# Kernel optimization log

Hardware: AMD Instinct MI355X
Metric: run time of the kernel (lower is better)

## Reference

```python
import jax, jax.numpy as jnp
import numpy as np

H, KV, D = 16, 4, 128
WIN = 512
EPS = 1e-6


def rms_norm(x, w):
    # x: [..., D]
    return x * jax.lax.rsqrt(jnp.mean(x * x, axis=-1, keepdims=True) + EPS) * w


def rotate_half(x):
    x1, x2 = jnp.split(x, 2, axis=-1)
    return jnp.concatenate([-x2, x1], axis=-1)


def setup_inputs() -> dict:
    key = jax.random.key(0)
    ks = jax.random.split(key, 8)
    B, L, hidden = 2, 2048, 2048
    x = jax.random.normal(ks[0], (B, L, hidden), jnp.float32)
    # realistic RoPE tables
    inv_freq = 1.0 / (10000.0 ** (np.arange(0, D, 2, dtype=np.float32) / D))
    t = np.arange(L, dtype=np.float32)
    freqs = np.outer(t, inv_freq)  # [L, D/2]
    emb = np.concatenate([freqs, freqs], axis=-1)  # [L, D]
    cos = jnp.asarray(np.cos(emb), jnp.float32)
    sin = jnp.asarray(np.sin(emb), jnp.float32)
    s = 0.02
    Wq = jax.random.normal(ks[1], (H * D, hidden), jnp.float32) * s
    Wk = jax.random.normal(ks[2], (KV * D, hidden), jnp.float32) * s
    Wv = jax.random.normal(ks[3], (KV * D, hidden), jnp.float32) * s
    Wo = jax.random.normal(ks[4], (hidden, H * D), jnp.float32) * s
    q_norm_w = jnp.ones((D,), jnp.float32)
    k_norm_w = jnp.ones((D,), jnp.float32)
    return {"x": x, "cos": cos, "sin": sin, "Wq": Wq, "Wk": Wk, "Wv": Wv,
            "Wo": Wo, "q_norm_w": q_norm_w, "k_norm_w": k_norm_w}


def reference(x, cos, sin, Wq, Wk, Wv, Wo, q_norm_w, k_norm_w):
    B, L, _ = x.shape
    # projections (torch Linear: y = x @ W.T)
    q = (x @ Wq.T).reshape(B, L, H, D)
    k = (x @ Wk.T).reshape(B, L, KV, D)
    v = (x @ Wv.T).reshape(B, L, KV, D)
    # QK RMSNorm, then [B, heads, L, D]
    q = jnp.transpose(rms_norm(q, q_norm_w), (0, 2, 1, 3))
    k = jnp.transpose(rms_norm(k, k_norm_w), (0, 2, 1, 3))
    v = jnp.transpose(v, (0, 2, 1, 3))
    # RoPE
    c = cos[None, None]  # [1,1,L,D]
    s = sin[None, None]
    q = q * c + rotate_half(q) * s
    k = k * c + rotate_half(k) * s
    # GQA repeat_interleave over head dim
    n_rep = H // KV
    k = jnp.repeat(k, n_rep, axis=1)
    v = jnp.repeat(v, n_rep, axis=1)
    # sliding-window additive bias [L, L]
    idx = jnp.arange(L)
    in_win = jnp.abs(idx[:, None] - idx[None, :]) <= WIN
    bias = jnp.where(in_win, 0.0, jnp.finfo(x.dtype).min).astype(x.dtype)
    # SDPA
    scale = 1.0 / jnp.sqrt(jnp.asarray(D, x.dtype))
    scores = jnp.einsum('bhqd,bhkd->bhqk', q, k) * scale + bias[None, None]
    attn = jax.nn.softmax(scores, axis=-1)
    out = jnp.einsum('bhqk,bhkd->bhqd', attn, v)  # [B,H,L,D]
    out = jnp.transpose(out, (0, 2, 1, 3)).reshape(B, L, H * D)
    return out @ Wo.T
```

## Files before the change

kernel.cpp:

```cpp
#include <hip/hip_runtime.h>
#include <hip/hip_bf16.h>


typedef unsigned short u16;
typedef unsigned int u32;
typedef __attribute__((ext_vector_type(8))) short bf16x8;
typedef __attribute__((ext_vector_type(4))) float f32x4;

#define AS1 __attribute__((address_space(1)))
#define AS3 __attribute__((address_space(3)))

__device__ __forceinline__ u16 f2b(float f) {
  union { float f; u32 u; } c; c.f = f;
  return (u16)((c.u + 0x8000u) >> 16);
}
__device__ __forceinline__ float b2f(u16 u) {
  union { u32 u; float f; } c; c.u = ((u32)u) << 16; return c.f;
}

__global__ __launch_bounds__(256) void cvt_all(const float* __restrict__ x,
                                               const float* __restrict__ wq,
                                               const float* __restrict__ wk,
                                               const float* __restrict__ wv,
                                               const float* __restrict__ wo,
                                               u16* __restrict__ xb,
                                               u16* __restrict__ wqkvb,
                                               u16* __restrict__ wob) {
  int blk = blockIdx.x;
  const float* s; u16* d; int off;
  if (blk < 8192)       { s = x;  d = xb;              off = blk * 1024; }
  else if (blk < 12288) { s = wq; d = wqkvb;           off = (blk - 8192) * 1024; }
  else if (blk < 13312) { s = wk; d = wqkvb + 4194304; off = (blk - 12288) * 1024; }
  else if (blk < 14336) { s = wv; d = wqkvb + 5242880; off = (blk - 13312) * 1024; }
  else                  { s = wo; d = wob;             off = (blk - 14336) * 1024; }
  int i = off + threadIdx.x * 4;
  float4 v = *(const float4*)(s + i);
  ushort4 o;
  o.x = f2b(v.x); o.y = f2b(v.y); o.z = f2b(v.z); o.w = f2b(v.w);
  *(ushort4*)(d + i) = o;
}

template<int F32OUT>
__global__ __launch_bounds__(256) void gemm_bt(const u16* __restrict__ A,
                                               const u16* __restrict__ Bm,
                                               void* __restrict__ C,
                                               int M, int N, int K) {
  __shared__ u16 As[128][64];
  __shared__ u16 Bs[128][64];
  const int tid  = threadIdx.x;
  const int w    = tid >> 6, lane = tid & 63, quad = lane >> 4, l16 = lane & 15;
  const int wm   = w >> 1, wn = w & 1;
  const int m0   = blockIdx.y * 128, n0 = blockIdx.x * 128;

  f32x4 zero = {0.f, 0.f, 0.f, 0.f};
  f32x4 acc[4][4];
#pragma unroll
  for (int i = 0; i < 4; i++)
#pragma unroll
    for (int j = 0; j < 4; j++) acc[i][j] = zero;

  const int srow = lane >> 3;
  const int swz8 = ((lane & 7) ^ (lane >> 3)) * 8;

  for (int k0 = 0; k0 < K; k0 += 64) {
#pragma unroll
    for (int p = 0; p < 4; ++p) {
      int row = p * 32 + w * 8 + srow;
      __builtin_amdgcn_global_load_lds(
          (const AS1 void*)(A + (size_t)(m0 + row) * K + k0 + swz8),
          (AS3 void*)((char*)&As[0][0] + p * 4096 + w * 1024), 16, 0, 0);
      __builtin_amdgcn_global_load_lds(
          (const AS1 void*)(Bm + (size_t)(n0 + row) * K + k0 + swz8),
          (AS3 void*)((char*)&Bs[0][0] + p * 4096 + w * 1024), 16, 0, 0);
    }
    __syncthreads();
#pragma unroll
    for (int kk = 0; kk < 64; kk += 32) {
      const int cs = ((kk >> 3) + quad) ^ (l16 & 7);
      bf16x8 af[4], bfr[4];
#pragma unroll
      for (int i = 0; i < 4; i++)
        af[i] = *(const bf16x8*)((const char*)&As[0][0] +
                                 (wm * 64 + i * 16 + l16) * 128 + cs * 16);
#pragma unroll
      for (int j = 0; j < 4; j++)
        bfr[j] = *(const bf16x8*)((const char*)&Bs[0][0] +
                                  (wn * 64 + j * 16 + l16) * 128 + cs * 16);
#pragma unroll
      for (int i = 0; i < 4; i++)
#pragma unroll
        for (int j = 0; j < 4; j++)
          acc[i][j] = __builtin_amdgcn_mfma_f32_16x16x32_bf16(af[i], bfr[j], acc[i][j], 0, 0, 0);
    }
    __syncthreads();
  }

#pragma unroll
  for (int i = 0; i < 4; i++) {
#pragma unroll
    for (int r = 0; r < 4; r++) {
      int gr = m0 + wm * 64 + i * 16 + quad * 4 + r;
#pragma unroll
      for (int j = 0; j < 4; j++) {
        int gc = n0 + wn * 64 + j * 16 + l16;
        if (F32OUT) ((float*)C)[(size_t)gr * N + gc] = acc[i][j][r];
        else        ((u16*)C)[(size_t)gr * N + gc]   = f2b(acc[i][j][r]);
      }
    }
  }
}

__global__ __launch_bounds__(256) void rmsrope(const u16* __restrict__ qkv,
                                               const float* __restrict__ cosT,
                                               const float* __restrict__ sinT,
                                               const float* __restrict__ qw,
                                               const float* __restrict__ kw,
                                               u16* __restrict__ qo,
                                               u16* __restrict__ ko) {
  int wid  = blockIdx.x * 4 + (threadIdx.x >> 6);
  int lane = threadIdx.x & 63;
  int r  = wid / 20;
  int hh = wid % 20;
  int b = r >> 11, l = r & 2047;
  int cb = hh < 16 ? hh * 128 : 2048 + (hh - 16) * 128;
  const u16* src = qkv + (size_t)r * 3072 + cb;
  float v0 = b2f(src[lane]);
  float v1 = b2f(src[lane + 64]);
  float ss = v0 * v0 + v1 * v1;
#pragma unroll
  for (int off = 1; off < 64; off <<= 1) ss += __shfl_xor(ss, off, 64);
  float inv = rsqrtf(ss * (1.0f / 128.0f) + 1e-6f);
  const float* wt = hh < 16 ? qw : kw;
  float n0 = v0 * inv * wt[lane];
  float n1 = v1 * inv * wt[lane + 64];
  float c0 = cosT[l * 128 + lane],      c1 = cosT[l * 128 + 64 + lane];
  float s0 = sinT[l * 128 + lane],      s1 = sinT[l * 128 + 64 + lane];
  float o0 = n0 * c0 - n1 * s0;
  float o1 = n1 * c1 + n0 * s1;
  const float qscale = 0.08838834764831845f * 1.4426950408889634f;
  u16* dst; size_t base;
  if (hh < 16) { dst = qo; base = ((size_t)(b * 16 + hh) * 2048 + l) * 128;
                 o0 *= qscale; o1 *= qscale; }
  else         { dst = ko; base = ((size_t)(b * 4 + (hh - 16)) * 2048 + l) * 128; }
  dst[base + lane]      = f2b(o0);
  dst[base + 64 + lane] = f2b(o1);
}

__global__ __launch_bounds__(256) void transpose_v(const u16* __restrict__ qkv,
                                                   u16* __restrict__ dst) {
  __shared__ u16 T[64][72];
  const int lt = blockIdx.x, dt = blockIdx.y, bh = blockIdx.z;
  const int b = bh >> 2, kv = bh & 3;
  const u16* s = qkv + ((size_t)(b * 2048 + lt * 64)) * 3072 + 2560 + kv * 128 + dt * 64;
  u16*       d = dst + (size_t)bh * 128 * 2048 + (size_t)dt * 64 * 2048 + lt * 64;
  const int t = threadIdx.x;
  const int row = t >> 3, c8 = (t & 7) * 8;
#pragma unroll
  for (int p = 0; p < 2; ++p)
    *(uint4*)&T[p * 32 + row][c8] = *(const uint4*)(s + (size_t)(p * 32 + row) * 3072 + c8);
  __syncthreads();
#pragma unroll
  for (int p = 0; p < 2; ++p) {
    int dr = p * 32 + row;
    u16 o[8];
#pragma unroll
    for (int j = 0; j < 8; ++j) o[j] = T[c8 + j][dr];
    *(uint4*)(d + (size_t)dr * 2048 + c8) = *(uint4*)o;
  }
}

__global__ __launch_bounds__(256) void flash_swa(const u16* __restrict__ Q,
                                                 const u16* __restrict__ Kg,
                                                 const u16* __restrict__ VTg,
                                                 u16* __restrict__ Og) {
  constexpr int L = 2048, D = 128;
  __shared__ u16 Ks[64][136];
  __shared__ u16 Vt[128][72];
  __shared__ u16 Ps[4][16][72];

  const int q0  = blockIdx.x * 128;
  const int h   = blockIdx.y;
  const int b   = blockIdx.z;
  const int tid = threadIdx.x;
  const int w = tid >> 6, lane = tid & 63, quad = lane >> 4, l16 = lane & 15;
  const int kvh = h >> 2;

  const u16* Qb  = Q   + (size_t)(b * 16 + h)  * L * D;
  const u16* Kb  = Kg  + (size_t)(b * 4 + kvh) * L * D;
  const u16* VTb = VTg + (size_t)(b * 4 + kvh) * D * L;

  bf16x8 qf[2][4];
#pragma unroll
  for (int g = 0; g < 2; ++g) {
    int qr = q0 + g * 64 + w * 16 + l16;
#pragma unroll
    for (int ks = 0; ks < 4; ++ks)
      qf[g][ks] = *(const bf16x8*)(Qb + (size_t)qr * D + ks * 32 + quad * 8);
  }

  f32x4 zero = {0.f, 0.f, 0.f, 0.f};
  f32x4 o[2][8];
#pragma unroll
  for (int g = 0; g < 2; ++g)
#pragma unroll
    for (int i = 0; i < 8; i++) o[g][i] = zero;
  float lrow[2] = {0.f, 0.f};

  int kt0   = q0 > 512 ? q0 - 512 : 0;
  int ktend = q0 + 128 + 512; if (ktend > L) ktend = L;

  for (int kt = kt0; kt < ktend; kt += 64) {
#pragma unroll
    for (int p = 0; p < 4; ++p) {
      int c = tid + p * 256;
      int row = c >> 4, c8 = (c & 15) * 8;
      *(uint4*)&Ks[row][c8] = *(const uint4*)(Kb + (size_t)(kt + row) * D + c8);
    }
#pragma unroll
    for (int p = 0; p < 4; ++p) {
      int c = tid + p * 256;
      int row = c >> 3, c8 = (c & 7) * 8;
      *(uint4*)&Vt[row][c8] = *(const uint4*)(VTb + (size_t)row * L + kt + c8);
    }
    __syncthreads();

#pragma unroll
    for (int g = 0; g < 2; ++g) {
      const int qg = q0 + g * 64;
      if (kt < qg - 512 || kt > qg + 512) continue;
      const int qi = qg + w * 16 + l16;

      f32x4 s[4];
#pragma unroll
      for (int ct = 0; ct < 4; ct++) s[ct] = zero;
#pragma unroll
      for (int ks = 0; ks < 4; ++ks) {
#pragma unroll
        for (int ct = 0; ct < 4; ++ct) {
          bf16x8 kf = *(const bf16x8*)&Ks[ct * 16 + l16][ks * 32 + quad * 8];
          s[ct] = __builtin_amdgcn_mfma_f32_16x16x32_bf16(kf, qf[g][ks], s[ct], 0, 0, 0);
        }
      }

      bool need_mask = (kt + 448 < qg) || (kt > qg + 448);
      float psum = 0.f;
#pragma unroll
      for (int ct = 0; ct < 4; ct++) {
        u16 ph[4];
#pragma unroll
        for (int r = 0; r < 4; r++) {
          float x = s[ct][r];
          if (need_mask) {
            int ki = kt + ct * 16 + quad * 4 + r;
            int dd = qi - ki; if (dd < 0) dd = -dd;
            if (dd > 512) x = -__builtin_inff();
          }
          float p = exp2f(x);
          psum += p;
          ph[r] = f2b(p);
        }
        uint2 pk;
        pk.x = (u32)ph[0] | ((u32)ph[1] << 16);
        pk.y = (u32)ph[2] | ((u32)ph[3] << 16);
        *(uint2*)&Ps[w][l16][ct * 16 + quad * 4] = pk;
      }
      psum += __shfl_xor(psum, 16, 64);
      psum += __shfl_xor(psum, 32, 64);
      lrow[g] += psum;

      bf16x8 pf[2];
#pragma unroll
      for (int ks2 = 0; ks2 < 2; ++ks2)
        pf[ks2] = *(const bf16x8*)&Ps[w][l16][ks2 * 32 + quad * 8];
#pragma unroll
      for (int dt = 0; dt < 8; ++dt) {
#pragma unroll
        for (int ks2 = 0; ks2 < 2; ++ks2) {
          bf16x8 vf = *(const bf16x8*)&Vt[dt * 16 + l16][ks2 * 32 + quad * 8];
          o[g][dt] = __builtin_amdgcn_mfma_f32_16x16x32_bf16(pf[ks2], vf, o[g][dt], 0, 0, 0);
        }
      }
    }
    __syncthreads();
  }

#pragma unroll
  for (int g = 0; g < 2; ++g) {
#pragma unroll
    for (int r = 0; r < 4; r++) {
      float lv  = __shfl(lrow[g], (lane & 48) + quad * 4 + r, 64);
      float inv = 1.0f / lv;
      int qr = q0 + g * 64 + w * 16 + quad * 4 + r;
      size_t base = ((size_t)(b * L + qr)) * 2048 + h * 128;
#pragma unroll
      for (int dt = 0; dt < 8; dt++)
        Og[base + dt * 16 + l16] = f2b(o[g][dt][r] * inv);
    }
  }
}

extern "C" void kernel_launch(void* const* d_in, const int* in_sizes, int n_in,
                              void* d_out, int out_size, void* d_ws, size_t ws_size,
                              hipStream_t stream) {
  const float* x    = (const float*)d_in[0];
  const float* cosT = (const float*)d_in[1];
  const float* sinT = (const float*)d_in[2];
  const float* Wq   = (const float*)d_in[3];
  const float* Wk   = (const float*)d_in[4];
  const float* Wv   = (const float*)d_in[5];
  const float* Wo   = (const float*)d_in[6];
  const float* qw   = (const float*)d_in[7];
  const float* kw   = (const float*)d_in[8];

  char* ws = (char*)d_ws;
  u16* x_bf    = (u16*)(ws + 0);
  u16* wqkv_bf = (u16*)(ws + 16777216);
  u16* wo_bf   = (u16*)(ws + 29360128);
  u16* qkv_bf  = (u16*)(ws + 37748736);
  u16* q_bf    = (u16*)(ws + 62914560);
  u16* k_bf    = (u16*)(ws + 79691776);
  u16* vt_bf   = wqkv_bf;
  u16* attn_bf = x_bf;

  cvt_all<<<18432, 256, 0, stream>>>(x, Wq, Wk, Wv, Wo, x_bf, wqkv_bf, wo_bf);
  gemm_bt<0><<<dim3(24, 32), 256, 0, stream>>>(x_bf, wqkv_bf, qkv_bf, 4096, 3072, 2048);
  rmsrope<<<20480, 256, 0, stream>>>(qkv_bf, cosT, sinT, qw, kw, q_bf, k_bf);
  transpose_v<<<dim3(32, 2, 8), 256, 0, stream>>>(qkv_bf, vt_bf);
  flash_swa<<<dim3(16, 16, 2), 256, 0, stream>>>(q_bf, k_bf, vt_bf, attn_bf);
  gemm_bt<1><<<dim3(16, 32), 256, 0, stream>>>(attn_bf, wo_bf, d_out, 4096, 2048, 2048);
}
```

Baseline: 315.7 us.

## Load K/V tiles via global_load_lds with XOR swizzle and share fragments across query groups

K and V^T tiles now go straight from global memory into LDS through global_load_lds, and the unpadded LDS layout uses an XOR swizzle to avoid bank conflicts. K and V fragments are read from LDS once per tile and reused by both 64-row query groups, where before each group read them separately. exp2f is swapped for the hardware exp2 builtin. The aim is to cut VGPR staging traffic and LDS reads. The cost is more registers held live for both groups' scores and P fragments.

```diff
diff --git a/kernel.cpp b/kernel.cpp
--- a/kernel.cpp
+++ b/kernel.cpp
@@ -9,6 +9,12 @@
 
 #define AS1 __attribute__((address_space(1)))
 #define AS3 __attribute__((address_space(3)))
+
+#if __has_builtin(__builtin_amdgcn_exp2f)
+#define EXP2(x) __builtin_amdgcn_exp2f(x)
+#else
+#define EXP2(x) exp2f(x)
+#endif
 
 __device__ __forceinline__ u16 f2b(float f) {
   union { float f; u32 u; } c; c.f = f;
@@ -174,8 +180,8 @@
                                                  const u16* __restrict__ VTg,
                                                  u16* __restrict__ Og) {
   constexpr int L = 2048, D = 128;
-  __shared__ u16 Ks[64][136];
-  __shared__ u16 Vt[128][72];
+  __shared__ u16 Ks[64 * 128];
+  __shared__ u16 Vt[128 * 64];
   __shared__ u16 Ps[4][16][72];
 
   const int q0  = blockIdx.x * 128;
@@ -209,39 +215,64 @@
   int kt0   = q0 > 512 ? q0 - 512 : 0;
   int ktend = q0 + 128 + 512; if (ktend > L) ktend = L;
 
+  const int krow_l = lane >> 4;
+  const int kcol_l = lane & 15;
+  const int vrow_l = lane >> 3;
+  const int vcol_l = lane & 7;
+
   for (int kt = kt0; kt < ktend; kt += 64) {
 #pragma unroll
     for (int p = 0; p < 4; ++p) {
-      int c = tid + p * 256;
-      int row = c >> 4, c8 = (c & 15) * 8;
-      *(uint4*)&Ks[row][c8] = *(const uint4*)(Kb + (size_t)(kt + row) * D + c8);
+      int row = p * 16 + w * 4 + krow_l;
+      int c   = kcol_l ^ (row & 7);
+      __builtin_amdgcn_global_load_lds(
+          (const AS1 void*)(Kb + (size_t)(kt + row) * D + c * 8),
+          (AS3 void*)((char*)Ks + p * 4096 + w * 1024), 16, 0, 0);
     }
 #pragma unroll
     for (int p = 0; p < 4; ++p) {
-      int c = tid + p * 256;
-      int row = c >> 3, c8 = (c & 7) * 8;
-      *(uint4*)&Vt[row][c8] = *(const uint4*)(VTb + (size_t)row * L + kt + c8);
+      int row = p * 32 + w * 8 + vrow_l;
+      int c   = vcol_l ^ (row & 7);
+      __builtin_amdgcn_global_load_lds(
+          (const AS1 void*)(VTb + (size_t)row * L + kt + c * 8),
+          (AS3 void*)((char*)Vt + p * 4096 + w * 1024), 16, 0, 0);
     }
     __syncthreads();
 
+    const bool act0 = (kt >= q0 - 512) && (kt <= q0 + 512);
+    const bool act1 = (kt >= q0 - 448);
+
+    f32x4 s[2][4];
+#pragma unroll
+    for (int g = 0; g < 2; ++g)
+#pragma unroll
+      for (int ct = 0; ct < 4; ct++) s[g][ct] = zero;
+#pragma unroll
+    for (int ks = 0; ks < 4; ++ks) {
+      bf16x8 kf[4];
+#pragma unroll
+      for (int ct = 0; ct < 4; ++ct) {
+        int cphys = ((ks * 4 + quad) ^ (l16 & 7));
+        kf[ct] = *(const bf16x8*)((const char*)Ks + (ct * 16 + l16) * 256 + cphys * 16);
+      }
+      if (act0) {
+#pragma unroll
+        for (int ct = 0; ct < 4; ++ct)
+          s[0][ct] = __builtin_amdgcn_mfma_f32_16x16x32_bf16(kf[ct], qf[0][ks], s[0][ct], 0, 0, 0);
+      }
+      if (act1) {
+#pragma unroll
+        for (int ct = 0; ct < 4; ++ct)
+          s[1][ct] = __builtin_amdgcn_mfma_f32_16x16x32_bf16(kf[ct], qf[1][ks], s[1][ct], 0, 0, 0);
+      }
+    }
+
+    bf16x8 pf[2][2];
 #pragma unroll
     for (int g = 0; g < 2; ++g) {
+      if (g == 0 ? !act0 : !act1) continue;
       const int qg = q0 + g * 64;
-      if (kt < qg - 512 || kt > qg + 512) continue;
       const int qi = qg + w * 16 + l16;
-
-      f32x4 s[4];
-#pragma unroll
-      for (int ct = 0; ct < 4; ct++) s[ct] = zero;
-#pragma unroll
-      for (int ks = 0; ks < 4; ++ks) {
-#pragma unroll
-        for (int ct = 0; ct < 4; ++ct) {
-          bf16x8 kf = *(const bf16x8*)&Ks[ct * 16 + l16][ks * 32 + quad * 8];
-          s[ct] = __builtin_amdgcn_mfma_f32_16x16x32_bf16(kf, qf[g][ks], s[ct], 0, 0, 0);
-        }
-      }
-
       bool need_mask = (kt + 448 < qg) || (kt > qg + 448);
       float psum = 0.f;
 #pragma unroll
@@ -249,13 +280,13 @@
         u16 ph[4];
 #pragma unroll
         for (int r = 0; r < 4; r++) {
-          float x = s[ct][r];
+          float x = s[g][ct][r];
           if (need_mask) {
             int ki = kt + ct * 16 + quad * 4 + r;
             int dd = qi - ki; if (dd < 0) dd = -dd;
             if (dd > 512) x = -__builtin_inff();
           }
-          float p = exp2f(x);
+          float p = EXP2(x);
           psum += p;
           ph[r] = f2b(p);
         }
@@ -267,18 +298,28 @@
       psum += __shfl_xor(psum, 16, 64);
       psum += __shfl_xor(psum, 32, 64);
       lrow[g] += psum;
-
-      bf16x8 pf[2];
 #pragma unroll
       for (int ks2 = 0; ks2 < 2; ++ks2)
-        pf[ks2] = *(const bf16x8*)&Ps[w][l16][ks2 * 32 + quad * 8];
-#pragma unroll
-      for (int dt = 0; dt < 8; ++dt) {
-#pragma unroll
-        for (int ks2 = 0; ks2 < 2; ++ks2) {
-          bf16x8 vf = *(const bf16x8*)&Vt[dt * 16 + l16][ks2 * 32 + quad * 8];
-          o[g][dt] = __builtin_amdgcn_mfma_f32_16x16x32_bf16(pf[ks2], vf, o[g][dt], 0, 0, 0);
-        }
+        pf[g][ks2] = *(const bf16x8*)&Ps[w][l16][ks2 * 32 + quad * 8];
+    }
+
+#pragma unroll
+    for (int dt = 0; dt < 8; ++dt) {
+      bf16x8 vf[2];
+#pragma unroll
+      for (int ks2 = 0; ks2 < 2; ++ks2) {
+        int cphys = ((ks2 * 4 + quad) ^ (l16 & 7));
+        vf[ks2] = *(const bf16x8*)((const char*)Vt + (dt * 16 + l16) * 128 + cphys * 16);
+      }
+      if (act0) {
+#pragma unroll
+        for (int ks2 = 0; ks2 < 2; ++ks2)
+          o[0][dt] = __builtin_amdgcn_mfma_f32_16x16x32_bf16(pf[0][ks2], vf[ks2], o[0][dt], 0, 0, 0);
+      }
+      if (act1) {
+#pragma unroll
+        for (int ks2 = 0; ks2 < 2; ++ks2)
+          o[1][dt] = __builtin_amdgcn_mfma_f32_16x16x32_bf16(pf[1][ks2], vf[ks2], o[1][dt], 0, 0, 0);
       }
     }
     __syncthreads();
```

After: 342.8 us. 8.6% more time.
